# Kernel optimization log

Measured on AMD Instinct MI355X. Metric: run time of the kernel, lower is better.

Reference implementation:

```python
import jax, jax.numpy as jnp
import numpy as np

B, S, I, H, O = 32, 2048, 128, 512, 128


def setup_inputs() -> dict:
    key = jax.random.key(0)
    ks = jax.random.split(key, 9)
    std = 1.0 / np.sqrt(H)
    u = lambda k, shape: jax.random.uniform(k, shape, jnp.float32, -std, std)
    return {
        "x": jax.random.normal(ks[0], (B, S, I), jnp.float32),
        # layer 0 cell: gates packed as [z; r; g]
        "wx0": u(ks[1], (3 * H, I)),
        "bx0": u(ks[2], (3 * H,)),
        "wh0": u(ks[3], (3 * H, H)),
        # layer 1 cell
        "wx1": u(ks[4], (3 * H, H)),
        "bx1": u(ks[5], (3 * H,)),
        "wh1": u(ks[6], (3 * H, H)),
        # output projection why
        "wy": u(ks[7], (O, H)),
        "by": u(ks[8], (O,)),
    }


def _gru_cell(x_t, h, wx, bx, wh):
    # x_t: (B, in), h: (B, H). One GEMM for x-gates, one for h-gates.
    gx = x_t @ wx.T + bx          # (B, 3H)
    gh = h @ wh.T                 # (B, 3H)
    xz, xr, xg = jnp.split(gx, 3, axis=-1)
    hz, hr, hg = jnp.split(gh, 3, axis=-1)
    z = jax.nn.sigmoid(xz + hz)
    r = jax.nn.sigmoid(xr + hr)
    g = jnp.tanh(xg + r * hg)
    return g + z * (h - g)


def reference(x, wx0, bx0, wh0, wx1, bx1, wh1, wy, by):
    h0 = jnp.zeros((B, H), x.dtype)
    h1 = jnp.zeros((B, H), x.dtype)

    def step(carry, x_t):
        h0, h1 = carry
        h0 = _gru_cell(x_t, h0, wx0, bx0, wh0)
        h1 = _gru_cell(h0, h1, wx1, bx1, wh1)
        y = h1 @ wy.T + by        # (B, O)
        return (h0, h1), y

    (h0, h1), ys = jax.lax.scan(step, (h0, h1), jnp.swapaxes(x, 0, 1))
    layer_output = jnp.swapaxes(ys, 0, 1)            # (B, S, O)
    hidden_state = jnp.stack([h0, h1], axis=1)       # (B, L, H)
    return layer_output, hidden_state
```

## Files before the change

### kernel.cpp

```cpp
#include <hip/hip_runtime.h>
#include <stdint.h>

#define BB 32
#define SS 2048
#define II 128
#define HH 512
#define OO 128

#define N0 16
#define N1 32
#define NYB 4
#define NBLK (N0 + N1 + NYB)
#define THREADS 256

#define SLOTS 8
#define SLOT_W (BB * HH)
#define H0_OFF 4096
#define H1_OFF (4096 + SLOTS * SLOT_W * 2)
#define WS_BYTES (4096 + 2 * SLOTS * SLOT_W * 2)

#define REDOFF    98304
#define LDS_BYTES (120 * 1024)

typedef __attribute__((ext_vector_type(8))) short short8;
typedef __attribute__((ext_vector_type(4))) float f32x4;
typedef __attribute__((ext_vector_type(4))) unsigned int u32x4;

__device__ __forceinline__ short f2bf(float f) {
  unsigned int u = __float_as_uint(f);
  u += 0x7fffu + ((u >> 16) & 1u);
  return (short)(u >> 16);
}
__device__ __forceinline__ float sigm(float v) { return 1.0f / (1.0f + __expf(-v)); }
__device__ __forceinline__ float tanhc(float v) {
  v = fminf(fmaxf(v, -15.0f), 15.0f);
  float e = __expf(2.0f * v);
  return (e - 1.0f) / (e + 1.0f);
}

#define LDG4T(dst_, p_) asm volatile("global_load_dwordx4 %0, %1, off sc1" : "=&v"(dst_) : "v"(p_))
#define LDGU(dst_, p_)  asm volatile("global_load_dword %0, %1, off sc1" : "=&v"(dst_) : "v"(p_))
#define STG2(p_, v_)    asm volatile("global_store_short %0, %1, off sc1" :: "v"(p_), "v"(v_))
#define STG4(p_, v_)    asm volatile("global_store_dword %0, %1, off sc1" :: "v"(p_), "v"(v_))
#define VDRAIN() do { \
  asm volatile("s_waitcnt vmcnt(0)" ::: "memory"); \
  __builtin_amdgcn_sched_barrier(0); \
} while (0)

__device__ __forceinline__ short8 mk_af8(u32x4 w) {
  short8 r;
  r[0] = (short)w[0]; r[1] = (short)(w[0] >> 16);
  r[2] = (short)w[1]; r[3] = (short)(w[1] >> 16);
  r[4] = (short)w[2]; r[5] = (short)(w[2] >> 16);
  r[6] = (short)w[3]; r[7] = (short)(w[3] >> 16);
  return r;
}
__device__ __forceinline__ short8 mk_af_x(float4 a, float4 b) {
  short8 r;
  r[0] = f2bf(a.x); r[1] = f2bf(a.y); r[2] = f2bf(a.z); r[3] = f2bf(a.w);
  r[4] = f2bf(b.x); r[5] = f2bf(b.y); r[6] = f2bf(b.z); r[7] = f2bf(b.w);
  return r;
}

__device__ __forceinline__ void poll_flags(const unsigned int* flags, int l,
                                           unsigned t0, unsigned t1, unsigned ty) {
  const unsigned thr = (l < 16) ? t0 : (l < 48) ? t1 : (l < 52) ? ty : 0u;
  const unsigned int* fp = flags + ((l < 52) ? l : 0);
  for (;;) {
    unsigned v;
    LDGU(v, fp);
    VDRAIN();
    if (__all((int)(v >= thr))) return;
    __builtin_amdgcn_s_sleep(4);
  }
}

__global__ __launch_bounds__(THREADS, 1)
void gru_persist(const float* __restrict__ x,
                 const float* __restrict__ wx0, const float* __restrict__ bx0,
                 const float* __restrict__ wh0,
                 const float* __restrict__ wx1, const float* __restrict__ bx1,
                 const float* __restrict__ wh1,
                 const float* __restrict__ wy,  const float* __restrict__ by,
                 float* __restrict__ out, unsigned char* __restrict__ ws)
{
  extern __shared__ char smem[];
  short8* ldsw = (short8*)smem;
  float*  red  = (float*)(smem + REDOFF);

  unsigned int*   flags = (unsigned int*)ws;
  unsigned short* pub0  = (unsigned short*)(ws + H0_OFF);
  unsigned short* pub1  = (unsigned short*)(ws + H1_OFF);

  const int tid = threadIdx.x;
  const int l   = tid & 63;
  const int wv  = tid >> 6;
  const int lr  = l & 15;
  const int lg  = l >> 4;
  const int bid = blockIdx.x;
  const int role = (bid < N0) ? 0 : (bid < N0 + N1) ? 1 : 2;

  if (role == 0) {
    for (int f = wv; f < 120; f += 4) {
      const int uh = f / 60, g = (f % 60) / 20, kt = f % 20;
      const int row = g * 512 + bid * 32 + uh * 16 + lr;
      const float* src = (kt < 4) ? (wx0 + (size_t)row * II + kt * 32 + lg * 8)
                                  : (wh0 + (size_t)row * HH + (kt - 4) * 32 + lg * 8);
      short8 v;
#pragma unroll
      for (int j = 0; j < 8; ++j) v[j] = f2bf(src[j]);
      ldsw[(f << 6) + l] = v;
    }
  } else if (role == 1) {
    const int ub = (bid - N0) * 16;
    for (int f = wv; f < 96; f += 4) {
      const int g = f >> 5, kt = f & 31;
      const int row = g * 512 + ub + lr;
      const float* src = (kt < 16) ? (wx1 + (size_t)row * HH + kt * 32 + lg * 8)
                                   : (wh1 + (size_t)row * HH + (kt - 16) * 32 + lg * 8);
      short8 v;
#pragma unroll
      for (int j = 0; j < 8; ++j) v[j] = f2bf(src[j]);
      ldsw[(f << 6) + l] = v;
    }
  } else {
    const int oy = (bid - N0 - N1) * 32;
    for (int f = wv; f < 32; f += 4) {
      const int nt = f >> 4, kt = f & 15;
      const int row = oy + nt * 16 + lr;
      const float* src = wy + (size_t)row * HH + kt * 32 + lg * 8;
      short8 v;
#pragma unroll
      for (int j = 0; j < 8; ++j) v[j] = f2bf(src[j]);
      ldsw[(f << 6) + l] = v;
    }
  }
  __syncthreads();

  if (role == 0) {
    const int mh  = wv & 1;
    const int uh  = wv >> 1;
    const int bA  = mh * 16 + lr;
    const int bC  = mh * 16 + lg * 4;
    const int u0w = bid * 32 + uh * 16;
    const int fb  = uh * 60;
    const float bz = bx0[u0w + lr], br = bx0[512 + u0w + lr], bg = bx0[1024 + u0w + lr];
    f32x4 hm = {0.f, 0.f, 0.f, 0.f};

    for (int p = 0; p < SS; ++p) {
      const float* xp = x + (size_t)bA * (SS * II) + (size_t)p * II + lg * 8;
      f32x4 aZ = {0,0,0,0}, aR = {0,0,0,0}, aG1 = {0,0,0,0}, aG2 = {0,0,0,0};
#pragma unroll
      for (int kt = 0; kt < 4; ++kt) {
        short8 af = mk_af_x(*(const float4*)(xp + kt * 32), *(const float4*)(xp + kt * 32 + 4));
        aZ  = __builtin_amdgcn_mfma_f32_16x16x32_bf16(af, ldsw[((fb + kt) << 6) + l], aZ, 0, 0, 0);
        aR  = __builtin_amdgcn_mfma_f32_16x16x32_bf16(af, ldsw[((fb + 20 + kt) << 6) + l], aR, 0, 0, 0);
        aG1 = __builtin_amdgcn_mfma_f32_16x16x32_bf16(af, ldsw[((fb + 40 + kt) << 6) + l], aG1, 0, 0, 0);
      }
      if (wv == 0) poll_flags(flags, l, (unsigned)p, (p >= 7) ? (unsigned)(p - 7) : 0u, 0u);
      __syncthreads();
      const unsigned short* pb = pub0 + (size_t)((p - 1) & 7) * SLOT_W + bA * HH + lg * 8;
      u32x4 pw[16];
#pragma unroll
      for (int i = 0; i < 16; ++i) LDG4T(pw[i], pb + i * 32);
      VDRAIN();
#pragma unroll
      for (int i = 0; i < 16; ++i) {
        const int kt = 4 + i;
        short8 af = mk_af8(pw[i]);
        aZ  = __builtin_amdgcn_mfma_f32_16x16x32_bf16(af, ldsw[((fb + kt) << 6) + l], aZ, 0, 0, 0);
        aR  = __builtin_amdgcn_mfma_f32_16x16x32_bf16(af, ldsw[((fb + 20 + kt) << 6) + l], aR, 0, 0, 0);
        aG2 = __builtin_amdgcn_mfma_f32_16x16x32_bf16(af, ldsw[((fb + 40 + kt) << 6) + l], aG2, 0, 0, 0);
      }
      unsigned short* po = pub0 + (size_t)(p & 7) * SLOT_W + u0w + lr;
#pragma unroll
      for (int r = 0; r < 4; ++r) {
        const float zz = sigm(aZ[r] + bz);
        const float rr = sigm(aR[r] + br);
        const float gg = tanhc(aG1[r] + bg + rr * aG2[r]);
        const float hn = gg + zz * (hm[r] - gg);
        hm[r] = hn;
        STG2(po + (size_t)(bC + r) * HH, (unsigned int)(unsigned short)f2bf(hn));
        if (p == SS - 1)
          out[(size_t)(BB * SS * OO) + (size_t)(bC + r) * (2 * HH) + u0w + lr] = hn;
      }
      VDRAIN();
      __syncthreads();
      if (tid == 0) STG4(flags + bid, (unsigned)(p + 1));
    }
  } else if (role == 1) {
    const int mh = wv & 1;
    const int kh = wv >> 1;
    const int bA = mh * 16 + lr;
    const int bC = mh * 16 + lg * 4;
    const int u0 = (bid - N0) * 16;
    float bz = 0.f, br = 0.f, bg = 0.f;
    if (kh == 0) { bz = bx1[u0 + lr]; br = bx1[512 + u0 + lr]; bg = bx1[1024 + u0 + lr]; }
    f32x4 hm = {0.f, 0.f, 0.f, 0.f};

    for (int p = 1; p <= SS; ++p) {
      if (wv == 0)
        poll_flags(flags, l, (unsigned)p, (unsigned)(p - 1), (p >= 7) ? (unsigned)(p - 7) : 0u);
      __syncthreads();
      f32x4 aZ = {0,0,0,0}, aR = {0,0,0,0}, aG1 = {0,0,0,0}, aG2 = {0,0,0,0};
      const int par = p & 1;
      if (kh == 0) {
        const unsigned short* pb0 = pub0 + (size_t)((p - 1) & 7) * SLOT_W + bA * HH + lg * 8;
        u32x4 pw[16];
#pragma unroll
        for (int i = 0; i < 16; ++i) LDG4T(pw[i], pb0 + i * 32);
        VDRAIN();
#pragma unroll
        for (int kt = 0; kt < 16; ++kt) {
          short8 af = mk_af8(pw[kt]);
          aZ  = __builtin_amdgcn_mfma_f32_16x16x32_bf16(af, ldsw[((0 * 32 + kt) << 6) + l], aZ, 0, 0, 0);
          aR  = __builtin_amdgcn_mfma_f32_16x16x32_bf16(af, ldsw[((1 * 32 + kt) << 6) + l], aR, 0, 0, 0);
          aG1 = __builtin_amdgcn_mfma_f32_16x16x32_bf16(af, ldsw[((2 * 32 + kt) << 6) + l], aG1, 0, 0, 0);
        }
      } else {
        const unsigned short* pb1 = pub1 + (size_t)((p - 2) & 7) * SLOT_W + bA * HH + lg * 8;
        u32x4 pw[16];
#pragma unroll
        for (int i = 0; i < 16; ++i) LDG4T(pw[i], pb1 + i * 32);
        VDRAIN();
#pragma unroll
        for (int i = 0; i < 16; ++i) {
          const int kt = 16 + i;
          short8 af = mk_af8(pw[i]);
          aZ  = __builtin_amdgcn_mfma_f32_16x16x32_bf16(af, ldsw[((0 * 32 + kt) << 6) + l], aZ, 0, 0, 0);
          aR  = __builtin_amdgcn_mfma_f32_16x16x32_bf16(af, ldsw[((1 * 32 + kt) << 6) + l], aR, 0, 0, 0);
          aG2 = __builtin_amdgcn_mfma_f32_16x16x32_bf16(af, ldsw[((2 * 32 + kt) << 6) + l], aG2, 0, 0, 0);
        }
#pragma unroll
        for (int r = 0; r < 4; ++r) {
          red[(((par * 2 + mh) * 3 + 0) * 4 + r) * 64 + l] = aZ[r];
          red[(((par * 2 + mh) * 3 + 1) * 4 + r) * 64 + l] = aR[r];
          red[(((par * 2 + mh) * 3 + 2) * 4 + r) * 64 + l] = aG2[r];
        }
      }
      __syncthreads();
      if (kh == 0) {
        unsigned short* po = pub1 + (size_t)((p - 1) & 7) * SLOT_W + u0 + lr;
#pragma unroll
        for (int r = 0; r < 4; ++r) {
          const float z2 = red[(((par * 2 + mh) * 3 + 0) * 4 + r) * 64 + l];
          const float r2 = red[(((par * 2 + mh) * 3 + 1) * 4 + r) * 64 + l];
          const float g2 = red[(((par * 2 + mh) * 3 + 2) * 4 + r) * 64 + l];
          const float zz = sigm(aZ[r] + z2 + bz);
          const float rr = sigm(aR[r] + r2 + br);
          const float gg = tanhc(aG1[r] + bg + rr * g2);
          const float hn = gg + zz * (hm[r] - gg);
          hm[r] = hn;
          STG2(po + (size_t)(bC + r) * HH, (unsigned int)(unsigned short)f2bf(hn));
          if (p == SS)
            out[(size_t)(BB * SS * OO) + (size_t)(bC + r) * (2 * HH) + HH + u0 + lr] = hn;
        }
        VDRAIN();
      }
      __syncthreads();
      if (tid == 0) STG4(flags + 16 + (bid - N0), (unsigned)p);
    }
  } else {
    const int mh  = wv & 1;
    const int ynt = wv >> 1;
    const int bA  = mh * 16 + lr;
    const int bC  = mh * 16 + lg * 4;
    const int yb  = bid - N0 - N1;
    const int oy  = yb * 32;
    const float byv = by[oy + ynt * 16 + lr];

    for (int p = 2; p <= SS + 1; ++p) {
      if (wv == 0) poll_flags(flags, l, 0u, (unsigned)(p - 1), 0u);
      __syncthreads();
      const unsigned short* pbV = pub1 + (size_t)((p - 2) & 7) * SLOT_W + bA * HH + lg * 8;
      u32x4 pw[16];
#pragma unroll
      for (int i = 0; i < 16; ++i) LDG4T(pw[i], pbV + i * 32);
      VDRAIN();
      __syncthreads();
      if (tid == 0) STG4(flags + 48 + yb, (unsigned)p);
      f32x4 acc = {0, 0, 0, 0};
#pragma unroll
      for (int kt = 0; kt < 16; ++kt)
        acc = __builtin_amdgcn_mfma_f32_16x16x32_bf16(mk_af8(pw[kt]), ldsw[((ynt * 16 + kt) << 6) + l], acc, 0, 0, 0);
#pragma unroll
      for (int r = 0; r < 4; ++r)
        out[(size_t)(bC + r) * (SS * OO) + (size_t)(p - 2) * OO + oy + ynt * 16 + lr] = acc[r] + byv;
    }
  }
}

extern "C" void kernel_launch(void* const* d_in, const int* in_sizes, int n_in,
                              void* d_out, int out_size, void* d_ws, size_t ws_size,
                              hipStream_t stream) {
  (void)in_sizes; (void)n_in; (void)out_size; (void)ws_size;
  const float* x   = (const float*)d_in[0];
  const float* wx0 = (const float*)d_in[1];
  const float* bx0 = (const float*)d_in[2];
  const float* wh0 = (const float*)d_in[3];
  const float* wx1 = (const float*)d_in[4];
  const float* bx1 = (const float*)d_in[5];
  const float* wh1 = (const float*)d_in[6];
  const float* wy  = (const float*)d_in[7];
  const float* by  = (const float*)d_in[8];
  float* out = (float*)d_out;

  hipMemsetAsync(d_ws, 0, WS_BYTES, stream);
  gru_persist<<<dim3(NBLK), dim3(THREADS), LDS_BYTES, stream>>>(
      x, wx0, bx0, wh0, wx1, bx1, wh1, wy, by, out, (unsigned char*)d_ws);
}
```

Measured before the change: 12.70 ms.

## Publish hidden states and flags via packed atomic swaps, drop poll sleep

Hidden-state publication now packs two bf16 values into one dword via a lane shuffle and writes them with global atomic swaps instead of per-lane short stores. Flag updates also use atomic swaps, and the s_sleep in the spin-poll loop is removed. The intent is to cut the per-step cross-block handoff latency of the persistent pipeline, since atomics resolve at the coherence point and polling reacts sooner. In exchange, busy polling adds memory traffic and the atomics may carry their own latency.

```diff
diff --git a/kernel.cpp b/kernel.cpp
--- a/kernel.cpp
+++ b/kernel.cpp
@@ -40,8 +40,7 @@
 
 #define LDG4T(dst_, p_) asm volatile("global_load_dwordx4 %0, %1, off sc1" : "=&v"(dst_) : "v"(p_))
 #define LDGU(dst_, p_)  asm volatile("global_load_dword %0, %1, off sc1" : "=&v"(dst_) : "v"(p_))
-#define STG2(p_, v_)    asm volatile("global_store_short %0, %1, off sc1" :: "v"(p_), "v"(v_))
-#define STG4(p_, v_)    asm volatile("global_store_dword %0, %1, off sc1" :: "v"(p_), "v"(v_))
+#define ATSW(p_, v_)    asm volatile("global_atomic_swap %0, %1, off sc1" :: "v"(p_), "v"(v_))
 #define VDRAIN() do { \
   asm volatile("s_waitcnt vmcnt(0)" ::: "memory"); \
   __builtin_amdgcn_sched_barrier(0); \
@@ -71,7 +70,6 @@
     LDGU(v, fp);
     VDRAIN();
     if (__all((int)(v >= thr))) return;
-    __builtin_amdgcn_s_sleep(4);
   }
 }
 
@@ -88,9 +86,9 @@
   short8* ldsw = (short8*)smem;
   float*  red  = (float*)(smem + REDOFF);
 
-  unsigned int*   flags = (unsigned int*)ws;
-  unsigned short* pub0  = (unsigned short*)(ws + H0_OFF);
-  unsigned short* pub1  = (unsigned short*)(ws + H1_OFF);
+  unsigned int*   flagsw = (unsigned int*)ws;
+  unsigned short* pub0   = (unsigned short*)(ws + H0_OFF);
+  unsigned short* pub1   = (unsigned short*)(ws + H1_OFF);
 
   const int tid = threadIdx.x;
   const int l   = tid & 63;
@@ -157,7 +155,7 @@
         aR  = __builtin_amdgcn_mfma_f32_16x16x32_bf16(af, ldsw[((fb + 20 + kt) << 6) + l], aR, 0, 0, 0);
         aG1 = __builtin_amdgcn_mfma_f32_16x16x32_bf16(af, ldsw[((fb + 40 + kt) << 6) + l], aG1, 0, 0, 0);
       }
-      if (wv == 0) poll_flags(flags, l, (unsigned)p, (p >= 7) ? (unsigned)(p - 7) : 0u, 0u);
+      if (wv == 0) poll_flags(flagsw, l, (unsigned)p, (p >= 7) ? (unsigned)(p - 7) : 0u, 0u);
       __syncthreads();
       const unsigned short* pb = pub0 + (size_t)((p - 1) & 7) * SLOT_W + bA * HH + lg * 8;
       u32x4 pw[16];
@@ -172,7 +170,6 @@
         aR  = __builtin_amdgcn_mfma_f32_16x16x32_bf16(af, ldsw[((fb + 20 + kt) << 6) + l], aR, 0, 0, 0);
         aG2 = __builtin_amdgcn_mfma_f32_16x16x32_bf16(af, ldsw[((fb + 40 + kt) << 6) + l], aG2, 0, 0, 0);
       }
-      unsigned short* po = pub0 + (size_t)(p & 7) * SLOT_W + u0w + lr;
 #pragma unroll
       for (int r = 0; r < 4; ++r) {
         const float zz = sigm(aZ[r] + bz);
@@ -180,13 +177,19 @@
         const float gg = tanhc(aG1[r] + bg + rr * aG2[r]);
         const float hn = gg + zz * (hm[r] - gg);
         hm[r] = hn;
-        STG2(po + (size_t)(bC + r) * HH, (unsigned int)(unsigned short)f2bf(hn));
+        const unsigned mine = (unsigned)(unsigned short)f2bf(hn);
+        const unsigned oth  = __shfl_xor(mine, 1);
+        if (!(lr & 1)) {
+          unsigned int* dp = (unsigned int*)(pub0 + (size_t)(p & 7) * SLOT_W
+                                             + (size_t)(bC + r) * HH + u0w + lr);
+          ATSW(dp, mine | (oth << 16));
+        }
         if (p == SS - 1)
           out[(size_t)(BB * SS * OO) + (size_t)(bC + r) * (2 * HH) + u0w + lr] = hn;
       }
       VDRAIN();
       __syncthreads();
-      if (tid == 0) STG4(flags + bid, (unsigned)(p + 1));
+      if (tid == 0) ATSW(flagsw + bid, (unsigned)(p + 1));
     }
   } else if (role == 1) {
     const int mh = wv & 1;
@@ -200,7 +203,7 @@
 
     for (int p = 1; p <= SS; ++p) {
       if (wv == 0)
-        poll_flags(flags, l, (unsigned)p, (unsigned)(p - 1), (p >= 7) ? (unsigned)(p - 7) : 0u);
+        poll_flags(flagsw, l, (unsigned)p, (unsigned)(p - 1), (p >= 7) ? (unsigned)(p - 7) : 0u);
       __syncthreads();
       f32x4 aZ = {0,0,0,0}, aR = {0,0,0,0}, aG1 = {0,0,0,0}, aG2 = {0,0,0,0};
       const int par = p & 1;
@@ -240,7 +243,6 @@
       }
       __syncthreads();
       if (kh == 0) {
-        unsigned short* po = pub1 + (size_t)((p - 1) & 7) * SLOT_W + u0 + lr;
 #pragma unroll
         for (int r = 0; r < 4; ++r) {
           const float z2 = red[(((par * 2 + mh) * 3 + 0) * 4 + r) * 64 + l];
@@ -251,14 +253,20 @@
           const float gg = tanhc(aG1[r] + bg + rr * g2);
           const float hn = gg + zz * (hm[r] - gg);
           hm[r] = hn;
-          STG2(po + (size_t)(bC + r) * HH, (unsigned int)(unsigned short)f2bf(hn));
+          const unsigned mine = (unsigned)(unsigned short)f2bf(hn);
+          const unsigned oth  = __shfl_xor(mine, 1);
+          if (!(lr & 1)) {
+            unsigned int* dp = (unsigned int*)(pub1 + (size_t)((p - 1) & 7) * SLOT_W
+                                               + (size_t)(bC + r) * HH + u0 + lr);
+            ATSW(dp, mine | (oth << 16));
+          }
           if (p == SS)
             out[(size_t)(BB * SS * OO) + (size_t)(bC + r) * (2 * HH) + HH + u0 + lr] = hn;
         }
         VDRAIN();
       }
       __syncthreads();
-      if (tid == 0) STG4(flags + 16 + (bid - N0), (unsigned)p);
+      if (tid == 0) ATSW(flagsw + 16 + (bid - N0), (unsigned)p);
     }
   } else {
     const int mh  = wv & 1;
@@ -270,7 +278,7 @@
     const float byv = by[oy + ynt * 16 + lr];
 
     for (int p = 2; p <= SS + 1; ++p) {
-      if (wv == 0) poll_flags(flags, l, 0u, (unsigned)(p - 1), 0u);
+      if (wv == 0) poll_flags(flagsw, l, 0u, (unsigned)(p - 1), 0u);
       __syncthreads();
       const unsigned short* pbV = pub1 + (size_t)((p - 2) & 7) * SLOT_W + bA * HH + lg * 8;
       u32x4 pw[16];
@@ -278,7 +286,7 @@
       for (int i = 0; i < 16; ++i) LDG4T(pw[i], pbV + i * 32);
       VDRAIN();
       __syncthreads();
-      if (tid == 0) STG4(flags + 48 + yb, (unsigned)p);
+      if (tid == 0) ATSW(flagsw + 48 + yb, (unsigned)p);
       f32x4 acc = {0, 0, 0, 0};
 #pragma unroll
       for (int kt = 0; kt < 16; ++kt)
```

After: 12.30 ms. -3.2%, faster.

## Replace block flag barriers with tagged per-element hidden-state publication

Applied to the files above, without the earlier changes.

Each hidden-state value is now published as a 32-bit word that holds the bf16 value in the upper half and the step tag in the lower half. Consumers spin on the data itself in two chunks instead of polling per-block flags behind __syncthreads. Per-wave progress flags are kept only to guard ring-slot reuse, and the ring shrinks from 8 slots to 4. The aim is to remove the store-drain, block barrier and flag round-trip from every step of the recurrence and to let partial work overlap. In exchange it doubles the size of the published state, and correctness now rests on tag matching and on the slot-reuse checks.

```diff
diff --git a/kernel.cpp b/kernel.cpp
--- a/kernel.cpp
+++ b/kernel.cpp
@@ -13,11 +13,14 @@
 #define NBLK (N0 + N1 + NYB)
 #define THREADS 256
 
-#define SLOTS 8
-#define SLOT_W (BB * HH)
-#define H0_OFF 4096
-#define H1_OFF (4096 + SLOTS * SLOT_W * 2)
-#define WS_BYTES (4096 + 2 * SLOTS * SLOT_W * 2)
+#define F0W_OFF 0
+#define F1A_OFF 256
+#define F1B_OFF 512
+#define FY_OFF  768
+#define SLOT_W  (BB * HH)
+#define PUB0_OFF 4096
+#define PUB1_OFF (4096 + 4 * SLOT_W * 4)
+#define WS_BYTES (4096 + 2 * 4 * SLOT_W * 4)
 
 #define REDOFF    98304
 #define LDS_BYTES (120 * 1024)
@@ -40,19 +43,18 @@
 
 #define LDG4T(dst_, p_) asm volatile("global_load_dwordx4 %0, %1, off sc1" : "=&v"(dst_) : "v"(p_))
 #define LDGU(dst_, p_)  asm volatile("global_load_dword %0, %1, off sc1" : "=&v"(dst_) : "v"(p_))
-#define STG2(p_, v_)    asm volatile("global_store_short %0, %1, off sc1" :: "v"(p_), "v"(v_))
 #define STG4(p_, v_)    asm volatile("global_store_dword %0, %1, off sc1" :: "v"(p_), "v"(v_))
 #define VDRAIN() do { \
   asm volatile("s_waitcnt vmcnt(0)" ::: "memory"); \
   __builtin_amdgcn_sched_barrier(0); \
 } while (0)
 
-__device__ __forceinline__ short8 mk_af8(u32x4 w) {
+__device__ __forceinline__ short8 mk_afT(u32x4 a, u32x4 b) {
   short8 r;
-  r[0] = (short)w[0]; r[1] = (short)(w[0] >> 16);
-  r[2] = (short)w[1]; r[3] = (short)(w[1] >> 16);
-  r[4] = (short)w[2]; r[5] = (short)(w[2] >> 16);
-  r[6] = (short)w[3]; r[7] = (short)(w[3] >> 16);
+  r[0] = (short)(a[0] >> 16); r[1] = (short)(a[1] >> 16);
+  r[2] = (short)(a[2] >> 16); r[3] = (short)(a[3] >> 16);
+  r[4] = (short)(b[0] >> 16); r[5] = (short)(b[1] >> 16);
+  r[6] = (short)(b[2] >> 16); r[7] = (short)(b[3] >> 16);
   return r;
 }
 __device__ __forceinline__ short8 mk_af_x(float4 a, float4 b) {
@@ -62,16 +64,19 @@
   return r;
 }
 
-__device__ __forceinline__ void poll_flags(const unsigned int* flags, int l,
-                                           unsigned t0, unsigned t1, unsigned ty) {
-  const unsigned thr = (l < 16) ? t0 : (l < 48) ? t1 : (l < 52) ? ty : 0u;
-  const unsigned int* fp = flags + ((l < 52) ? l : 0);
+__device__ __forceinline__ void chunk_wait(const unsigned int* base, int k0,
+                                           unsigned tag, u32x4* pw) {
   for (;;) {
-    unsigned v;
-    LDGU(v, fp);
+#pragma unroll
+    for (int i = 0; i < 8; ++i) {
+      LDG4T(pw[2 * i],     base + (k0 + i) * 32);
+      LDG4T(pw[2 * i + 1], base + (k0 + i) * 32 + 4);
+    }
     VDRAIN();
-    if (__all((int)(v >= thr))) return;
-    __builtin_amdgcn_s_sleep(4);
+    unsigned a = 0xFFFFFFFFu;
+#pragma unroll
+    for (int i = 0; i < 16; ++i) a &= pw[i][0] & pw[i][1] & pw[i][2] & pw[i][3];
+    if (__all((int)((a & 0xFFFFu) == tag))) return;
   }
 }
 
@@ -88,9 +93,12 @@
   short8* ldsw = (short8*)smem;
   float*  red  = (float*)(smem + REDOFF);
 
-  unsigned int*   flags = (unsigned int*)ws;
-  unsigned short* pub0  = (unsigned short*)(ws + H0_OFF);
-  unsigned short* pub1  = (unsigned short*)(ws + H1_OFF);
+  unsigned int* f0w  = (unsigned int*)(ws + F0W_OFF);
+  unsigned int* f1a  = (unsigned int*)(ws + F1A_OFF);
+  unsigned int* f1b  = (unsigned int*)(ws + F1B_OFF);
+  unsigned int* fyf  = (unsigned int*)(ws + FY_OFF);
+  unsigned int* pub0 = (unsigned int*)(ws + PUB0_OFF);
+  unsigned int* pub1 = (unsigned int*)(ws + PUB1_OFF);
 
   const int tid = threadIdx.x;
   const int l   = tid & 63;
@@ -145,34 +153,60 @@
     const int u0w = bid * 32 + uh * 16;
     const int fb  = uh * 60;
     const float bz = bx0[u0w + lr], br = bx0[512 + u0w + lr], bg = bx0[1024 + u0w + lr];
+    unsigned int* myf = f0w + bid * 4 + wv;
     f32x4 hm = {0.f, 0.f, 0.f, 0.f};
+    u32x4 pw[16];
 
     for (int p = 0; p < SS; ++p) {
+      unsigned gf0, gf1;
+      LDGU(gf0, f0w + l);
+      LDGU(gf1, f1a + l);
       const float* xp = x + (size_t)bA * (SS * II) + (size_t)p * II + lg * 8;
+      float4 xa[4], xb[4];
+#pragma unroll
+      for (int t = 0; t < 4; ++t) {
+        xa[t] = *(const float4*)(xp + t * 32);
+        xb[t] = *(const float4*)(xp + t * 32 + 4);
+      }
       f32x4 aZ = {0,0,0,0}, aR = {0,0,0,0}, aG1 = {0,0,0,0}, aG2 = {0,0,0,0};
+      if (p > 0) {
+        const unsigned int* pbase = pub0 + (size_t)((p - 1) & 3) * SLOT_W + bA * 512 + lg * 8;
+        chunk_wait(pbase, 0, (unsigned)p, pw);
+#pragma unroll
+        for (int i = 0; i < 8; ++i) {
+          short8 af = mk_afT(pw[2 * i], pw[2 * i + 1]);
+          aZ  = __builtin_amdgcn_mfma_f32_16x16x32_bf16(af, ldsw[((fb + 4 + i) << 6) + l], aZ, 0, 0, 0);
+          aR  = __builtin_amdgcn_mfma_f32_16x16x32_bf16(af, ldsw[((fb + 24 + i) << 6) + l], aR, 0, 0, 0);
+          aG2 = __builtin_amdgcn_mfma_f32_16x16x32_bf16(af, ldsw[((fb + 44 + i) << 6) + l], aG2, 0, 0, 0);
+        }
+        chunk_wait(pbase, 8, (unsigned)p, pw);
+#pragma unroll
+        for (int i = 0; i < 8; ++i) {
+          short8 af = mk_afT(pw[2 * i], pw[2 * i + 1]);
+          aZ  = __builtin_amdgcn_mfma_f32_16x16x32_bf16(af, ldsw[((fb + 12 + i) << 6) + l], aZ, 0, 0, 0);
+          aR  = __builtin_amdgcn_mfma_f32_16x16x32_bf16(af, ldsw[((fb + 32 + i) << 6) + l], aR, 0, 0, 0);
+          aG2 = __builtin_amdgcn_mfma_f32_16x16x32_bf16(af, ldsw[((fb + 52 + i) << 6) + l], aG2, 0, 0, 0);
+        }
+        if (l == 0) STG4(myf, (unsigned)p);
+      }
 #pragma unroll
       for (int kt = 0; kt < 4; ++kt) {
-        short8 af = mk_af_x(*(const float4*)(xp + kt * 32), *(const float4*)(xp + kt * 32 + 4));
+        short8 af = mk_af_x(xa[kt], xb[kt]);
         aZ  = __builtin_amdgcn_mfma_f32_16x16x32_bf16(af, ldsw[((fb + kt) << 6) + l], aZ, 0, 0, 0);
         aR  = __builtin_amdgcn_mfma_f32_16x16x32_bf16(af, ldsw[((fb + 20 + kt) << 6) + l], aR, 0, 0, 0);
         aG1 = __builtin_amdgcn_mfma_f32_16x16x32_bf16(af, ldsw[((fb + 40 + kt) << 6) + l], aG1, 0, 0, 0);
       }
-      if (wv == 0) poll_flags(flags, l, (unsigned)p, (p >= 7) ? (unsigned)(p - 7) : 0u, 0u);
-      __syncthreads();
-      const unsigned short* pb = pub0 + (size_t)((p - 1) & 7) * SLOT_W + bA * HH + lg * 8;
-      u32x4 pw[16];
-#pragma unroll
-      for (int i = 0; i < 16; ++i) LDG4T(pw[i], pb + i * 32);
-      VDRAIN();
-#pragma unroll
-      for (int i = 0; i < 16; ++i) {
-        const int kt = 4 + i;
-        short8 af = mk_af8(pw[i]);
-        aZ  = __builtin_amdgcn_mfma_f32_16x16x32_bf16(af, ldsw[((fb + kt) << 6) + l], aZ, 0, 0, 0);
-        aR  = __builtin_amdgcn_mfma_f32_16x16x32_bf16(af, ldsw[((fb + 20 + kt) << 6) + l], aR, 0, 0, 0);
-        aG2 = __builtin_amdgcn_mfma_f32_16x16x32_bf16(af, ldsw[((fb + 40 + kt) << 6) + l], aG2, 0, 0, 0);
-      }
-      unsigned short* po = pub0 + (size_t)(p & 7) * SLOT_W + u0w + lr;
+      if (p >= 4) {
+        const unsigned thr = (unsigned)(p - 3);
+        while (!__all((int)((gf0 >= thr) & (gf1 >= thr)))) {
+          __builtin_amdgcn_s_sleep(2);
+          LDGU(gf0, f0w + l);
+          LDGU(gf1, f1a + l);
+          VDRAIN();
+        }
+      }
+      unsigned int* po = pub0 + (size_t)(p & 3) * SLOT_W + u0w + lr;
+      const unsigned tagO = (unsigned)(p + 1);
 #pragma unroll
       for (int r = 0; r < 4; ++r) {
         const float zz = sigm(aZ[r] + bz);
@@ -180,13 +214,10 @@
         const float gg = tanhc(aG1[r] + bg + rr * aG2[r]);
         const float hn = gg + zz * (hm[r] - gg);
         hm[r] = hn;
-        STG2(po + (size_t)(bC + r) * HH, (unsigned int)(unsigned short)f2bf(hn));
+        STG4(po + (size_t)(bC + r) * 512, ((unsigned)(unsigned short)f2bf(hn) << 16) | tagO);
         if (p == SS - 1)
           out[(size_t)(BB * SS * OO) + (size_t)(bC + r) * (2 * HH) + u0w + lr] = hn;
       }
-      VDRAIN();
-      __syncthreads();
-      if (tid == 0) STG4(flags + bid, (unsigned)(p + 1));
     }
   } else if (role == 1) {
     const int mh = wv & 1;
@@ -196,51 +227,83 @@
     const int u0 = (bid - N0) * 16;
     float bz = 0.f, br = 0.f, bg = 0.f;
     if (kh == 0) { bz = bx1[u0 + lr]; br = bx1[512 + u0 + lr]; bg = bx1[1024 + u0 + lr]; }
+    unsigned int* myfa = f1a + (bid - N0) * 2 + mh;
+    unsigned int* myfb = f1b + (bid - N0) * 2 + mh;
     f32x4 hm = {0.f, 0.f, 0.f, 0.f};
-
-    for (int p = 1; p <= SS; ++p) {
-      if (wv == 0)
-        poll_flags(flags, l, (unsigned)p, (unsigned)(p - 1), (p >= 7) ? (unsigned)(p - 7) : 0u);
-      __syncthreads();
+    u32x4 pw[16];
+
+    for (int q = 1; q <= SS; ++q) {
+      const int par = q & 1;
       f32x4 aZ = {0,0,0,0}, aR = {0,0,0,0}, aG1 = {0,0,0,0}, aG2 = {0,0,0,0};
-      const int par = p & 1;
-      if (kh == 0) {
-        const unsigned short* pb0 = pub0 + (size_t)((p - 1) & 7) * SLOT_W + bA * HH + lg * 8;
-        u32x4 pw[16];
-#pragma unroll
-        for (int i = 0; i < 16; ++i) LDG4T(pw[i], pb0 + i * 32);
-        VDRAIN();
-#pragma unroll
-        for (int kt = 0; kt < 16; ++kt) {
-          short8 af = mk_af8(pw[kt]);
-          aZ  = __builtin_amdgcn_mfma_f32_16x16x32_bf16(af, ldsw[((0 * 32 + kt) << 6) + l], aZ, 0, 0, 0);
-          aR  = __builtin_amdgcn_mfma_f32_16x16x32_bf16(af, ldsw[((1 * 32 + kt) << 6) + l], aR, 0, 0, 0);
-          aG1 = __builtin_amdgcn_mfma_f32_16x16x32_bf16(af, ldsw[((2 * 32 + kt) << 6) + l], aG1, 0, 0, 0);
-        }
-      } else {
-        const unsigned short* pb1 = pub1 + (size_t)((p - 2) & 7) * SLOT_W + bA * HH + lg * 8;
-        u32x4 pw[16];
-#pragma unroll
-        for (int i = 0; i < 16; ++i) LDG4T(pw[i], pb1 + i * 32);
-        VDRAIN();
-#pragma unroll
-        for (int i = 0; i < 16; ++i) {
-          const int kt = 16 + i;
-          short8 af = mk_af8(pw[i]);
-          aZ  = __builtin_amdgcn_mfma_f32_16x16x32_bf16(af, ldsw[((0 * 32 + kt) << 6) + l], aZ, 0, 0, 0);
-          aR  = __builtin_amdgcn_mfma_f32_16x16x32_bf16(af, ldsw[((1 * 32 + kt) << 6) + l], aR, 0, 0, 0);
-          aG2 = __builtin_amdgcn_mfma_f32_16x16x32_bf16(af, ldsw[((2 * 32 + kt) << 6) + l], aG2, 0, 0, 0);
-        }
+      unsigned gfb, gfy;
+      if (kh == 1) {
+        if (q >= 2) {
+          const unsigned int* b1 = pub1 + (size_t)((q - 2) & 3) * SLOT_W + bA * 512 + lg * 8;
+          chunk_wait(b1, 0, (unsigned)(q - 1), pw);
+#pragma unroll
+          for (int i = 0; i < 8; ++i) {
+            const int kt = 16 + i;
+            short8 af = mk_afT(pw[2 * i], pw[2 * i + 1]);
+            aZ  = __builtin_amdgcn_mfma_f32_16x16x32_bf16(af, ldsw[((0 * 32 + kt) << 6) + l], aZ, 0, 0, 0);
+            aR  = __builtin_amdgcn_mfma_f32_16x16x32_bf16(af, ldsw[((1 * 32 + kt) << 6) + l], aR, 0, 0, 0);
+            aG2 = __builtin_amdgcn_mfma_f32_16x16x32_bf16(af, ldsw[((2 * 32 + kt) << 6) + l], aG2, 0, 0, 0);
+          }
+          chunk_wait(b1, 8, (unsigned)(q - 1), pw);
+#pragma unroll
+          for (int i = 0; i < 8; ++i) {
+            const int kt = 24 + i;
+            short8 af = mk_afT(pw[2 * i], pw[2 * i + 1]);
+            aZ  = __builtin_amdgcn_mfma_f32_16x16x32_bf16(af, ldsw[((0 * 32 + kt) << 6) + l], aZ, 0, 0, 0);
+            aR  = __builtin_amdgcn_mfma_f32_16x16x32_bf16(af, ldsw[((1 * 32 + kt) << 6) + l], aR, 0, 0, 0);
+            aG2 = __builtin_amdgcn_mfma_f32_16x16x32_bf16(af, ldsw[((2 * 32 + kt) << 6) + l], aG2, 0, 0, 0);
+          }
+        }
+        if (l == 0) STG4(myfb, (unsigned)q);
 #pragma unroll
         for (int r = 0; r < 4; ++r) {
           red[(((par * 2 + mh) * 3 + 0) * 4 + r) * 64 + l] = aZ[r];
           red[(((par * 2 + mh) * 3 + 1) * 4 + r) * 64 + l] = aR[r];
           red[(((par * 2 + mh) * 3 + 2) * 4 + r) * 64 + l] = aG2[r];
         }
+      } else {
+        LDGU(gfb, f1b + l);
+        LDGU(gfy, fyf + (l & 15));
+        const unsigned int* b0 = pub0 + (size_t)((q - 1) & 3) * SLOT_W + bA * 512 + lg * 8;
+        chunk_wait(b0, 0, (unsigned)q, pw);
+#pragma unroll
+        for (int kt = 0; kt < 8; ++kt) {
+          short8 af = mk_afT(pw[2 * kt], pw[2 * kt + 1]);
+          aZ  = __builtin_amdgcn_mfma_f32_16x16x32_bf16(af, ldsw[((0 * 32 + kt) << 6) + l], aZ, 0, 0, 0);
+          aR  = __builtin_amdgcn_mfma_f32_16x16x32_bf16(af, ldsw[((1 * 32 + kt) << 6) + l], aR, 0, 0, 0);
+          aG1 = __builtin_amdgcn_mfma_f32_16x16x32_bf16(af, ldsw[((2 * 32 + kt) << 6) + l], aG1, 0, 0, 0);
+        }
+        chunk_wait(b0, 8, (unsigned)q, pw);
+#pragma unroll
+        for (int i = 0; i < 8; ++i) {
+          const int kt = 8 + i;
+          short8 af = mk_afT(pw[2 * i], pw[2 * i + 1]);
+          aZ  = __builtin_amdgcn_mfma_f32_16x16x32_bf16(af, ldsw[((0 * 32 + kt) << 6) + l], aZ, 0, 0, 0);
+          aR  = __builtin_amdgcn_mfma_f32_16x16x32_bf16(af, ldsw[((1 * 32 + kt) << 6) + l], aR, 0, 0, 0);
+          aG1 = __builtin_amdgcn_mfma_f32_16x16x32_bf16(af, ldsw[((2 * 32 + kt) << 6) + l], aG1, 0, 0, 0);
+        }
+        if (l == 0) STG4(myfa, (unsigned)q);
       }
       __syncthreads();
       if (kh == 0) {
-        unsigned short* po = pub1 + (size_t)((p - 1) & 7) * SLOT_W + u0 + lr;
+        if (q >= 4) {
+          const unsigned thr = (unsigned)(q - 3);
+          for (;;) {
+            bool ok = ((l < 64 ? gfb : 0xFFFFFFFFu) >= thr) & ((gfy >= thr) | (0));
+            if (__all((int)(((gfb >= thr)) & (gfy >= thr)))) break;
+            __builtin_amdgcn_s_sleep(2);
+            LDGU(gfb, f1b + l);
+            LDGU(gfy, fyf + (l & 15));
+            VDRAIN();
+            (void)ok;
+          }
+        }
+        unsigned int* po = pub1 + (size_t)((q - 1) & 3) * SLOT_W + u0 + lr;
+        const unsigned tagO = (unsigned)q;
 #pragma unroll
         for (int r = 0; r < 4; ++r) {
           const float z2 = red[(((par * 2 + mh) * 3 + 0) * 4 + r) * 64 + l];
@@ -251,14 +314,11 @@
           const float gg = tanhc(aG1[r] + bg + rr * g2);
           const float hn = gg + zz * (hm[r] - gg);
           hm[r] = hn;
-          STG2(po + (size_t)(bC + r) * HH, (unsigned int)(unsigned short)f2bf(hn));
-          if (p == SS)
+          STG4(po + (size_t)(bC + r) * 512, ((unsigned)(unsigned short)f2bf(hn) << 16) | tagO);
+          if (q == SS)
             out[(size_t)(BB * SS * OO) + (size_t)(bC + r) * (2 * HH) + HH + u0 + lr] = hn;
         }
-        VDRAIN();
-      }
-      __syncthreads();
-      if (tid == 0) STG4(flags + 16 + (bid - N0), (unsigned)p);
+      }
     }
   } else {
     const int mh  = wv & 1;
@@ -268,21 +328,23 @@
     const int yb  = bid - N0 - N1;
     const int oy  = yb * 32;
     const float byv = by[oy + ynt * 16 + lr];
+    unsigned int* myfy = fyf + yb * 4 + wv;
+    u32x4 pw[16];
 
     for (int p = 2; p <= SS + 1; ++p) {
-      if (wv == 0) poll_flags(flags, l, 0u, (unsigned)(p - 1), 0u);
-      __syncthreads();
-      const unsigned short* pbV = pub1 + (size_t)((p - 2) & 7) * SLOT_W + bA * HH + lg * 8;
-      u32x4 pw[16];
-#pragma unroll
-      for (int i = 0; i < 16; ++i) LDG4T(pw[i], pbV + i * 32);
-      VDRAIN();
-      __syncthreads();
-      if (tid == 0) STG4(flags + 48 + yb, (unsigned)p);
-      f32x4 acc = {0, 0, 0, 0};
-#pragma unroll
-      for (int kt = 0; kt < 16; ++kt)
-        acc = __builtin_amdgcn_mfma_f32_16x16x32_bf16(mk_af8(pw[kt]), ldsw[((ynt * 16 + kt) << 6) + l], acc, 0, 0, 0);
+      const unsigned int* bV = pub1 + (size_t)((p - 2) & 3) * SLOT_W + bA * 512 + lg * 8;
+      f32x4 acc = {0.f, 0.f, 0.f, 0.f};
+      chunk_wait(bV, 0, (unsigned)(p - 1), pw);
+#pragma unroll
+      for (int kt = 0; kt < 8; ++kt)
+        acc = __builtin_amdgcn_mfma_f32_16x16x32_bf16(mk_afT(pw[2 * kt], pw[2 * kt + 1]),
+                                                      ldsw[((ynt * 16 + kt) << 6) + l], acc, 0, 0, 0);
+      chunk_wait(bV, 8, (unsigned)(p - 1), pw);
+#pragma unroll
+      for (int i = 0; i < 8; ++i)
+        acc = __builtin_amdgcn_mfma_f32_16x16x32_bf16(mk_afT(pw[2 * i], pw[2 * i + 1]),
+                                                      ldsw[((ynt * 16 + 8 + i) << 6) + l], acc, 0, 0, 0);
+      if (l == 0) STG4(myfy, (unsigned)p);
 #pragma unroll
       for (int r = 0; r < 4; ++r)
         out[(size_t)(bC + r) * (SS * OO) + (size_t)(p - 2) * OO + oy + ynt * 16 + lr] = acc[r] + byv;
```

Result: slower. 13.64 ms (+7.5%).
